# Kernel optimization log

Hardware: AMD Instinct MI355X
Metric: run time of the kernel (lower is better)

Reference implementation:

```python
import jax, jax.numpy as jnp
import numpy as np
import math

SPARSITY = 0.5
EPS = 1e-5


def _quant(x, bit, after_relu):
    # mirrors torch quantize_per_tensor math; straight-through (torch mutates x.data)
    def q(x):
        mx, mn = x.max(), x.min()
        scale = (mx - mn) / (2 ** bit - 1)
        if after_relu:
            ir = jnp.clip(jnp.round(x / scale), 0.0, 2 ** bit - 1)
            return ir * scale
        zp_min = jnp.floor(mn / scale)
        return (jnp.round((x - mn) / scale) + zp_min) * scale
    return x + jax.lax.stop_gradient(q(x) - x)


def _subnet(scores, k):
    # GetSubnet: top-k mask of |scores| with straight-through gradient
    s = jnp.abs(scores)
    flat = s.ravel()
    j = int((1.0 - k) * flat.size)
    order = jnp.argsort(flat)
    mask = jnp.zeros_like(flat).at[order[j:]].set(1.0).reshape(s.shape)
    return jax.lax.stop_gradient(mask - s) + s


def _scale(hw_one, fan_in):
    std = math.sqrt(2.0) / math.sqrt(fan_in * 0.5)
    return hw_one.mean() / std


def _blend_w(scores, sign, hw_one, hw_zero):
    m = _subnet(scores, SPARSITY)
    return sign * (hw_one[0] * m + hw_zero[0] * (1.0 - m))


def _conv(x, w):
    return jax.lax.conv_general_dilated(x, w, (1, 1), 'VALID',
                                        dimension_numbers=('NCHW', 'OIHW', 'NCHW'))


def _maxpool2(x):
    return jax.lax.reduce_window(x, -jnp.inf, jax.lax.max,
                                 (1, 1, 2, 2), (1, 1, 2, 2), 'VALID')


def _bn(x):
    m = x.mean((0, 2, 3), keepdims=True)
    v = x.var((0, 2, 3), keepdims=True)
    return (x - m) / jnp.sqrt(v + EPS)


def setup_inputs() -> dict:
    key = jax.random.key(0)
    ks = jax.random.split(key, 16)
    B = 4096
    shapes = {
        '1': (64, 1, 3, 3),
        '2': (16, 64, 3, 3),
        '3': (128, 400),
        '4': (10, 128),
    }
    inp = {'x': jax.random.normal(ks[0], (B, 1, 28, 28), dtype=jnp.float32)}
    i = 1
    for name, shp in shapes.items():
        inp['scores' + name] = jax.random.normal(ks[i], shp, dtype=jnp.float32); i += 1
        inp['sign' + name] = jnp.sign(jax.random.normal(ks[i], shp, dtype=jnp.float32)); i += 1
        inp['hw' + name + '_one'] = jax.random.uniform(ks[i], (1,) + shp, dtype=jnp.float32); i += 1
        # hw_zero: small "off" conductances
        inp['hw' + name + '_zero'] = 0.05 * jax.random.uniform(jax.random.fold_in(ks[i], 1), (1,) + shp, dtype=jnp.float32)
    inp['qb'] = 8
    return inp


def reference(x, scores1, sign1, hw1_one, hw1_zero,
              scores2, sign2, hw2_one, hw2_zero,
              scores3, sign3, hw3_one, hw3_zero,
              scores4, sign4, hw4_one, hw4_zero, qb):
    x = _maxpool2(x)
    x = _quant(x, qb, False)
    # conv1 (fan_in = 1*3*3 = 9)
    w1 = _blend_w(scores1, sign1, hw1_one, hw1_zero)
    x = _conv(x, w1) / _scale(hw1_one, 9)
    x = jax.nn.relu(_bn(x))
    x = _quant(x, qb, True)
    # conv2 (fan_in = 64*9 = 576)
    w2 = _blend_w(scores2, sign2, hw2_one, hw2_zero)
    x = _conv(x, w2) / _scale(hw2_one, 576)
    x = _maxpool2(x)
    x = jax.nn.relu(_bn(x))
    x = _quant(x, qb, True)
    x = x.reshape(x.shape[0], -1)  # [B, 400]
    # fc1 (fan_in = 400)
    w3 = _blend_w(scores3, sign3, hw3_one, hw3_zero)
    x = (x @ w3.T) / _scale(hw3_one, 400)
    x = jax.nn.relu(x)
    x = _quant(x, qb, True)
    # fc2 (fan_in = 128)
    w4 = _blend_w(scores4, sign4, hw4_one, hw4_zero)
    x = (x @ w4.T) / _scale(hw4_one, 128)
    return jax.nn.log_softmax(x, axis=1)
```

## Files before the change

### kernel.cpp

```cpp
#include <hip/hip_runtime.h>
#include <hip/hip_bf16.h>
#include <math.h>

#define DEV __device__ __forceinline__

constexpr int BATCH = 4096;
constexpr int NBA = 512;
constexpr int NBB = 1024;
constexpr int NBC = 4096;
constexpr int NBE = 512;
constexpr int NBW = 16;

constexpr size_t OFF_POOLED = 0;
constexpr size_t OFF_Y2P = OFF_POOLED + (size_t)BATCH*196;
constexpr size_t OFF_ST1 = OFF_Y2P;
constexpr size_t OFF_H3  = OFF_Y2P + (size_t)BATCH*400;
constexpr size_t OFF_ST2 = OFF_H3;
constexpr size_t OFF_W2  = OFF_H3 + (size_t)BATCH*128;
constexpr size_t OFF_W3  = OFF_W2 + 9216;
constexpr size_t OFF_W4  = OFF_W3 + 51200;
constexpr size_t OFF_WSC = OFF_W4 + 1280;
constexpr size_t OFF_BN1 = OFF_WSC + 4;
constexpr size_t OFF_BN2 = OFF_BN1 + 256;
constexpr size_t OFF_GMM = OFF_BN2 + 64;
constexpr size_t OFF_ONS = OFF_GMM + 8;
constexpr size_t OFF_T   = OFF_ONS + 16;
constexpr size_t OFF_MMA = OFF_T + 4;
constexpr size_t OFF_HIST= OFF_MMA + 1024;
constexpr size_t OFF_W1M = OFF_HIST + 32768;
constexpr size_t OFF_SEL = OFF_W1M + 2048;
constexpr size_t OFF_H2G = OFF_SEL + 8;
constexpr size_t OFF_H3G = OFF_H2G + 4096;

typedef __attribute__((ext_vector_type(8))) short bf16x8;
typedef __attribute__((ext_vector_type(4))) float f32x4;

struct InPtrs {
  const float* x;
  const float* sc[4];
  const float* sg[4];
  const float* on[4];
  const float* ze[4];
  const int* qb;
};

__constant__ const int KW_L[16]  ={0,1,1,2,2,2,2,2,2,2,2,2,2,2,2,3};
__constant__ const int KW_S[16]  ={0,0,1,0,1,2,3,4,5,6,7,8,9,10,11,0};
__constant__ const int KW_NB[4]  ={1,2,12,1};
__constant__ const int KW_N[4]   ={576,9216,51200,1280};
__constant__ const int KW_FAN[4] ={9,576,400,128};
__constant__ const int KW_BW0[4] ={0,1,3,15};
__constant__ const int KW_BW1[4] ={1,3,15,16};

DEV unsigned fenc(float f){ unsigned u=__float_as_uint(f); return (u&0x80000000u)? ~u : (u|0x80000000u); }
DEV float fdec(unsigned e){ return __uint_as_float((e&0x80000000u)? (e&0x7fffffffu) : ~e); }
DEV unsigned short f2bf(float f){ unsigned u=__float_as_uint(f); return (unsigned short)((u + 0x7fffu + ((u>>16)&1u))>>16); }

DEV float blk_sum(float v, float* red, int t){
  red[t]=v; __syncthreads();
  for (int s=128;s>0;s>>=1){ if(t<s) red[t]+=red[t+s]; __syncthreads(); }
  float r=red[0]; __syncthreads();
  return r;
}
DEV float blk_min(float v, float* red, int t){
  red[t]=v; __syncthreads();
  for (int s=128;s>0;s>>=1){ if(t<s) red[t]=fminf(red[t],red[t+s]); __syncthreads(); }
  float r=red[0]; __syncthreads();
  return r;
}
DEV float blk_max(float v, float* red, int t){
  red[t]=v; __syncthreads();
  for (int s=128;s>0;s>>=1){ if(t<s) red[t]=fmaxf(red[t],red[t+s]); __syncthreads(); }
  float r=red[0]; __syncthreads();
  return r;
}

DEV int2 find256(const int* hist, int nbins, int kk, int t, int* suf, int* sh2){
  const int G=nbins>>8;
  const int lo=t*G;
  int g=0;
  for (int b=0;b<G;++b) g+=hist[lo+b];
  suf[t]=g; __syncthreads();
  for (int s=1;s<256;s<<=1){
    int add=(t+s<256)?suf[t+s]:0;
    __syncthreads();
    suf[t]+=add;
    __syncthreads();
  }
  const int S=suf[t];
  const int Snext=(t<255)?suf[t+1]:0;
  if (S>=kk && Snext<kk){
    int c2=Snext;
    for (int b=lo+G-1;b>=lo;--b){
      c2+=hist[b];
      if (c2>=kk){ sh2[0]=b; sh2[1]=kk-(c2-hist[b]); break; }
    }
  }
  __syncthreads();
  int2 r=make_int2(sh2[0],sh2[1]);
  __syncthreads();
  return r;
}

DEV void build_pat(unsigned* PAT, const unsigned short* qxs, int t){
  for (int pos=t; pos<144; pos+=256){
    int py=(pos*171)>>11;
    int px=pos-py*12;
    const unsigned short* q0=qxs+py*16+px;
    unsigned e0=q0[0],  e1=q0[1],  e2=q0[2];
    unsigned e3=q0[16], e4=q0[17], e5=q0[18];
    unsigned e6=q0[32], e7=q0[33], e8=q0[34];
    uint4* dst=(uint4*)(PAT+pos*20);
    dst[0]=make_uint4(e0|(e1<<16), e2|(e3<<16), e4|(e5<<16), e6|(e7<<16));
    dst[1]=make_uint4(e8, 0u, 0u, 0u);
    dst[2]=make_uint4(0u,0u,0u,0u);
    dst[3]=make_uint4(0u,0u,0u,0u);
  }
}

__global__ __launch_bounds__(256) void ka_kernel(InPtrs in, float* __restrict__ ws){
  const int t=threadIdx.x, blk=blockIdx.x;
  __shared__ int h[2048];
  __shared__ float red[256];
  if (blk<NBA){
    if (blk==0){
      unsigned* Z=(unsigned*)(ws+OFF_H2G);
      for (int i=t;i<8192;i+=256) Z[i]=0u;
    }
    const float* x=in.x;
    float* pooled=ws+OFF_POOLED;
    float lmn=3.4e38f, lmx=-3.4e38f;
    if (t<196){
      const int oy=(t*2341)>>15;
      const int ox=t-oy*14;
      const float* xb=x+(size_t)blk*8*784+oy*56+ox*2;
      #pragma unroll
      for (int im=0; im<8; ++im){
        const float* px=xb+im*784;
        float m=fmaxf(fmaxf(px[0],px[1]),fmaxf(px[28],px[29]));
        pooled[(size_t)(blk*8+im)*196+t]=m;
        lmn=fminf(lmn,m); lmx=fmaxf(lmx,m);
      }
    }
    float bmn=blk_min(lmn,red,t);
    float bmx=blk_max(lmx,red,t);
    if (t==0){ ws[OFF_MMA+blk*2]=bmn; ws[OFF_MMA+blk*2+1]=bmx; }
  } else {
    const int bw=blk-NBA;
    const int L=KW_L[bw], s=KW_S[bw], nb=KW_NB[L];
    const int n4=KW_N[L]>>2;
    const int lo=(int)(((long long)n4*s)/nb), hi=(int)(((long long)n4*(s+1))/nb);
    const float4* sc4=(const float4*)in.sc[L];
    const float4* on4=(const float4*)in.on[L];
    for (int i=t;i<2048;i+=256) h[i]=0;
    __syncthreads();
    float onsum=0.f;
    for (int i=lo+t;i<hi;i+=256){
      float4 v=sc4[i];
      atomicAdd(&h[(__float_as_uint(v.x)&0x7fffffffu)>>20],1);
      atomicAdd(&h[(__float_as_uint(v.y)&0x7fffffffu)>>20],1);
      atomicAdd(&h[(__float_as_uint(v.z)&0x7fffffffu)>>20],1);
      atomicAdd(&h[(__float_as_uint(v.w)&0x7fffffffu)>>20],1);
      float4 o=on4[i];
      onsum+=(o.x+o.y)+(o.z+o.w);
    }
    __syncthreads();
    unsigned* GH=(unsigned*)(ws+OFF_HIST);
    for (int i=t;i<2048;i+=256) GH[bw*2048+i]=(unsigned)h[i];
    float S=blk_sum(onsum,red,t);
    if (t==0) ws[OFF_ONS+bw]=S;
  }
}

__global__ __launch_bounds__(256) void kw2a_kernel(float* __restrict__ ws){
  const int t=threadIdx.x, L=blockIdx.x;
  __shared__ int hist[2048];
  __shared__ int suf[256];
  __shared__ int sh2[2];
  __shared__ float redm[256], redx[256];
  if (L==0){
    float a0=ws[OFF_MMA+2*t],       a1=ws[OFF_MMA+2*(t+256)];
    float b0=ws[OFF_MMA+2*t+1],     b1=ws[OFF_MMA+2*(t+256)+1];
    redm[t]=fminf(a0,a1); redx[t]=fmaxf(b0,b1);
    __syncthreads();
    for (int s=128;s>0;s>>=1){
      if (t<s){ redm[t]=fminf(redm[t],redm[t+s]); redx[t]=fmaxf(redx[t],redx[t+s]); }
      __syncthreads();
    }
    unsigned* U=(unsigned*)(ws+OFF_GMM);
    if (t==0){ U[0]=fenc(redm[0]); U[1]=fenc(redx[0]); }
    if (t>=2 && t<8) U[t]=(t&1)? 0u : 0xFFFFFFFFu;
    unsigned* z=(unsigned*)(ws+OFF_W1M);
    for (int i=t;i<2048;i+=256) z[i]=0u;
    __syncthreads();
  }
  const unsigned* GH=(const unsigned*)(ws+OFF_HIST);
  for (int i=t;i<2048;i+=256){
    int s=0;
    for (int bw=KW_BW0[L]; bw<KW_BW1[L]; ++bw) s+=(int)GH[bw*2048+i];
    hist[i]=s;
  }
  __syncthreads();
  int2 f1=find256(hist,2048,KW_N[L]>>1,t,suf,sh2);
  if (t==0){
    unsigned* SEL=(unsigned*)(ws+OFF_SEL);
    SEL[L*2]=(unsigned)f1.x; SEL[L*2+1]=(unsigned)f1.y;
  }
}

__global__ __launch_bounds__(256) void kwp2_kernel(InPtrs in, float* __restrict__ ws){
  const int t=threadIdx.x, bw=blockIdx.x;
  const int L=KW_L[bw], s=KW_S[bw], nb=KW_NB[L];
  const int n4=KW_N[L]>>2;
  const int lo=(int)(((long long)n4*s)/nb), hi=(int)(((long long)n4*(s+1))/nb);
  const unsigned b0=((const unsigned*)(ws+OFF_SEL))[L*2];
  const float4* sc4=(const float4*)in.sc[L];
  unsigned* GH2=(unsigned*)(ws+OFF_H2G)+L*1024;
  for (int i=lo+t;i<hi;i+=256){
    float4 v=sc4[i];
    unsigned ux=__float_as_uint(v.x)&0x7fffffffu;
    unsigned uy=__float_as_uint(v.y)&0x7fffffffu;
    unsigned uz=__float_as_uint(v.z)&0x7fffffffu;
    unsigned uw=__float_as_uint(v.w)&0x7fffffffu;
    if ((ux>>20)==b0) atomicAdd(&GH2[(ux>>10)&1023u],1u);
    if ((uy>>20)==b0) atomicAdd(&GH2[(uy>>10)&1023u],1u);
    if ((uz>>20)==b0) atomicAdd(&GH2[(uz>>10)&1023u],1u);
    if ((uw>>20)==b0) atomicAdd(&GH2[(uw>>10)&1023u],1u);
  }
}

__global__ __launch_bounds__(256) void kwp3_kernel(InPtrs in, float* __restrict__ ws){
  const int t=threadIdx.x, bw=blockIdx.x;
  const int L=KW_L[bw], s=KW_S[bw], nb=KW_NB[L];
  const int n4=KW_N[L]>>2;
  const int lo=(int)(((long long)n4*s)/nb), hi=(int)(((long long)n4*(s+1))/nb);
  const unsigned* SEL=(const unsigned*)(ws+OFF_SEL);
  const unsigned b0=SEL[L*2]; const int r1=(int)SEL[L*2+1];
  __shared__ int hist[1024];
  __shared__ int suf[256];
  __shared__ int sh2[2];
  const unsigned* GH2=(const unsigned*)(ws+OFF_H2G)+L*1024;
  for (int i=t;i<1024;i+=256) hist[i]=(int)GH2[i];
  __syncthreads();
  int2 f2=find256(hist,1024,r1,t,suf,sh2);
  const unsigned pre=(b0<<10)|(unsigned)f2.x;
  const float4* sc4=(const float4*)in.sc[L];
  unsigned* GH3=(unsigned*)(ws+OFF_H3G)+L*1024;
  for (int i=lo+t;i<hi;i+=256){
    float4 v=sc4[i];
    unsigned ux=__float_as_uint(v.x)&0x7fffffffu;
    unsigned uy=__float_as_uint(v.y)&0x7fffffffu;
    unsigned uz=__float_as_uint(v.z)&0x7fffffffu;
    unsigned uw=__float_as_uint(v.w)&0x7fffffffu;
    if ((ux>>10)==pre) atomicAdd(&GH3[ux&1023u],1u);
    if ((uy>>10)==pre) atomicAdd(&GH3[uy&1023u],1u);
    if ((uz>>10)==pre) atomicAdd(&GH3[uz&1023u],1u);
    if ((uw>>10)==pre) atomicAdd(&GH3[uw&1023u],1u);
  }
}

__global__ __launch_bounds__(256) void kw3_kernel(InPtrs in, float* __restrict__ ws){
  const int t=threadIdx.x, bw=blockIdx.x;
  const int L=KW_L[bw], s=KW_S[bw], nb=KW_NB[L];
  const int n4=KW_N[L]>>2;
  const int lo=(int)(((long long)n4*s)/nb), hi=(int)(((long long)n4*(s+1))/nb);
  const unsigned* SEL=(const unsigned*)(ws+OFF_SEL);
  const unsigned b0=SEL[L*2]; const int r1=(int)SEL[L*2+1];
  __shared__ int hist[1024];
  __shared__ int suf[256];
  __shared__ int sh2[2];
  const unsigned* GH2=(const unsigned*)(ws+OFF_H2G)+L*1024;
  for (int i=t;i<1024;i+=256) hist[i]=(int)GH2[i];
  __syncthreads();
  int2 f2=find256(hist,1024,r1,t,suf,sh2);
  const unsigned pre=(b0<<10)|(unsigned)f2.x;
  const int r2=f2.y;
  __syncthreads();
  const unsigned* GH3=(const unsigned*)(ws+OFF_H3G)+L*1024;
  for (int i=t;i<1024;i+=256) hist[i]=(int)GH3[i];
  __syncthreads();
  int2 f3=find256(hist,1024,r2,t,suf,sh2);
  const unsigned T=(pre<<10)|(unsigned)f3.x;
  if (s==0 && t==0){
    float os=0.f;
    for (int b=KW_BW0[L]; b<KW_BW1[L]; ++b) os+=ws[OFF_ONS+b];
    ws[OFF_WSC+L]=(os/(float)KW_N[L])*sqrtf((float)KW_FAN[L])*0.5f;
  }
  const float4* sc4=(const float4*)in.sc[L];
  const float4* sg4=(const float4*)in.sg[L];
  const float4* on4=(const float4*)in.on[L];
  const float4* ze4=(const float4*)in.ze[L];
  float* wout=ws+OFF_W4;
  unsigned* W3Fu=(unsigned*)(ws+OFF_W3);
  unsigned short* W1F=(unsigned short*)(ws+OFF_W1M);
  unsigned short* W2F=(unsigned short*)(ws+OFF_W2);
  for (int i4=lo+t;i4<hi;i4+=256){
    float4 sv4=sc4[i4], g=sg4[i4], o=on4[i4], z=ze4[i4];
    float sv[4]={sv4.x,sv4.y,sv4.z,sv4.w}, gv[4]={g.x,g.y,g.z,g.w};
    float ov[4]={o.x,o.y,o.z,o.w}, zv[4]={z.x,z.y,z.z,z.w};
    #pragma unroll
    for (int j=0;j<4;++j){
      int i=i4*4+j;
      unsigned u=__float_as_uint(sv[j])&0x7fffffffu;
      float w=gv[j]*((u>=T)? ov[j] : zv[j]);
      if (L==0){
        int oc=i/9; int k=i-oc*9;
        int ocT=oc>>4, ocL=oc&15, quad=k>>3, kj=k&7;
        unsigned short hb=f2bf(w);
        float lo2=w-__uint_as_float((unsigned)hb<<16);
        W1F[((((ocT*2+0)*4+quad)*16+ocL)<<3)+kj]=hb;
        W1F[((((ocT*2+1)*4+quad)*16+ocL)<<3)+kj]=f2bf(lo2);
      } else if (L==1){
        int oc=i/576; int r=i-oc*576; int ic=r/9; int kp=r-ic*9;
        int ss=ic>>5, rem=ic&31, quad=rem>>3, kj=rem&7;
        unsigned short hb=f2bf(w);
        float lo2=w-__uint_as_float((unsigned)hb<<16);
        W2F[(((((kp*2+ss)*2+0)*4+quad)*16+oc)<<3)+kj]=hb;
        W2F[(((((kp*2+ss)*2+1)*4+quad)*16+oc)<<3)+kj]=f2bf(lo2);
      } else if (L==2){
        int oc=i/400; int kk=i-oc*400;
        unsigned short hb=f2bf(w);
        float lo2=w-__uint_as_float((unsigned)hb<<16);
        unsigned short lb=f2bf(lo2);
        int ct=oc>>4, l15=oc&15;
        unsigned idx=((unsigned)((kk>>4)*8+ct)*64u + (unsigned)(((kk>>2)&3)*16+l15))*4u + (unsigned)(kk&3);
        W3Fu[idx]=(unsigned)hb | ((unsigned)lb<<16);
      } else {
        wout[i]=w;
      }
    }
  }
}

__global__ __launch_bounds__(256) void kb_kernel(InPtrs in, const float* __restrict__ wsr, float* __restrict__ wsw){
  const int t=threadIdx.x, blk=blockIdx.x;
  __shared__ unsigned short qxs[256];
  __shared__ __align__(16) unsigned PAT[2880];
  __shared__ float xw[1024];
  const float* pooled=wsr+OFF_POOLED;
  const unsigned* U=(const unsigned*)(wsr+OFF_GMM);
  const float mn0=fdec(U[0]);
  const float mx0=fdec(U[1]);
  const float lvf=(float)((1<<in.qb[0])-1);
  const float s0=(mx0-mn0)/lvf, inv_s0=1.0f/s0, zp0=floorf(mn0/s0);
  const float sv=s0/wsr[OFF_WSC+0];
  const int w=t>>6, lane=t&63, l15=lane&15, quad=lane>>4;
  const unsigned short* W1F=(const unsigned short*)(wsr+OFF_W1M);
  bf16x8 bh[4], bl[4];
  #pragma unroll
  for (int ocT=0; ocT<4; ++ocT){
    bh[ocT]=*(const bf16x8*)(W1F+(((ocT*2+0)*64+lane)<<3));
    bl[ocT]=*(const bf16x8*)(W1F+(((ocT*2+1)*64+lane)<<3));
  }
  float sum[4], sq[4], mn[4], mx[4];
  #pragma unroll
  for (int i=0;i<4;++i){ sum[i]=0.f; sq[i]=0.f; mn[i]=3.4e38f; mx[i]=-3.4e38f; }
  for (int img=0; img<4; ++img){
    if (t<224){
      int row=t>>4, col=t&15;
      float q=0.f;
      if (col<14){ float xx=pooled[(size_t)(blk*4+img)*196+row*14+col]; q=rintf((xx-mn0)*inv_s0)+zp0; }
      qxs[t]=(unsigned short)(__float_as_uint(q)>>16);
    }
    __syncthreads();
    build_pat(PAT,qxs,t);
    __syncthreads();
    const unsigned short* PATu=(const unsigned short*)PAT;
    #pragma unroll
    for (int ocT=0; ocT<4; ++ocT){
      for (int tl=w; tl<9; tl+=4){
        bf16x8 a=*(const bf16x8*)(PATu+(tl*16+l15)*40+quad*8);
        f32x4 acc=(f32x4){0.f,0.f,0.f,0.f};
        acc=__builtin_amdgcn_mfma_f32_16x16x32_bf16(a,bh[ocT],acc,0,0,0);
        acc=__builtin_amdgcn_mfma_f32_16x16x32_bf16(a,bl[ocT],acc,0,0,0);
        #pragma unroll
        for (int r=0;r<4;++r){
          float v=acc[r];
          sum[ocT]+=v; sq[ocT]=fmaf(v,v,sq[ocT]);
          mn[ocT]=fminf(mn[ocT],v); mx[ocT]=fmaxf(mx[ocT],v);
        }
      }
    }
    __syncthreads();
  }
  #pragma unroll
  for (int ocT=0; ocT<4; ++ocT){
    float s=sum[ocT], q2=sq[ocT], a=mn[ocT], b=mx[ocT];
    #pragma unroll
    for (int d=16;d<64;d<<=1){
      s+=__shfl_xor(s,d);
      q2+=__shfl_xor(q2,d);
      a=fminf(a,__shfl_xor(a,d));
      b=fmaxf(b,__shfl_xor(b,d));
    }
    if (quad==0){
      float* p=xw+((w*4+ocT)*16+l15)*4;
      p[0]=s; p[1]=q2; p[2]=a; p[3]=b;
    }
  }
  __syncthreads();
  if (t<64){
    float s=0.f,q2=0.f,a=3.4e38f,b=-3.4e38f;
    #pragma unroll
    for (int w2=0;w2<4;++w2){
      const float* p=xw+((w2*4+(t>>4))*16+(t&15))*4;
      s+=p[0]; q2+=p[1]; a=fminf(a,p[2]); b=fmaxf(b,p[3]);
    }
    float* p=wsw+OFF_ST1+((size_t)t*NBB+blk)*4;
    p[0]=s*sv; p[1]=q2*sv*sv; p[2]=a*sv; p[3]=b*sv;
  }
}

__global__ __launch_bounds__(256) void kstat_kernel(const float* __restrict__ wsr, float* __restrict__ wsw,
                                                    unsigned long long inoff, int nparts, float Nf,
                                                    unsigned long long outoff, int mmslot){
  const int c=blockIdx.x, t=threadIdx.x;
  __shared__ float red[256];
  const float* p=wsr+inoff+(size_t)c*nparts*4;
  float sum=0.f,sq=0.f,mn=3.4e38f,mx=-3.4e38f;
  for (int i=t;i<nparts;i+=256){
    sum+=p[i*4]; sq+=p[i*4+1];
    mn=fminf(mn,p[i*4+2]); mx=fmaxf(mx,p[i*4+3]);
  }
  float S=blk_sum(sum,red,t);
  float Q=blk_sum(sq,red,t);
  float MN=blk_min(mn,red,t);
  float MX=blk_max(mx,red,t);
  if (t==0){
    float mean=S/Nf;
    float var=fmaxf(Q/Nf-mean*mean,0.f);
    float sd=sqrtf(var+1e-5f);
    float* o=wsw+outoff+c*4;
    float tmn=(MN-mean)/sd, tmx=(MX-mean)/sd;
    o[0]=mean; o[1]=sd; o[2]=tmn; o[3]=tmx;
    unsigned* U=(unsigned*)(wsw+OFF_GMM);
    atomicMin(&U[mmslot],fenc(tmn));
    atomicMax(&U[mmslot+1],fenc(tmx));
  }
}

__global__ __launch_bounds__(256) void kc_kernel(InPtrs in, const float* __restrict__ wsr, float* __restrict__ wsw){
  const int t=threadIdx.x, blk=blockIdx.x;
  __shared__ unsigned short qxs[256];
  __shared__ __align__(16) unsigned PATBUF[3328];
  __shared__ __align__(16) unsigned short actA[144*88];
  __shared__ float sA2[64], sB2[64];
  unsigned* PAT=PATBUF;
  float (*c2sP)[16][104]=(float(*)[16][104])PATBUF;
  const float* pooled=wsr+OFF_POOLED;
  const unsigned* U=(const unsigned*)(wsr+OFF_GMM);
  const float mn0=fdec(U[0]);
  const float mx0=fdec(U[1]);
  const float rmn=fdec(U[2]);
  const float rmx=fdec(U[3]);
  const float lvf=(float)((1<<in.qb[0])-1);
  const float s0=(mx0-mn0)/lvf, inv_s0=1.0f/s0, zp0=floorf(mn0/s0);
  const float s1w=wsr[OFF_WSC+0], s2w=wsr[OFF_WSC+1];
  const float s2=(fmaxf(rmx,0.f)-fmaxf(rmn,0.f))/lvf;
  const float inv_s2=1.0f/s2;
  const float g2=s2/s2w;
  if (t<64){
    float m=wsr[OFF_BN1+t*4], sd=wsr[OFF_BN1+t*4+1];
    sA2[t]=s0/(s1w*sd)*inv_s2;
    sB2[t]=(-m/sd)*inv_s2;
  }
  if (t<224){
    int row=t>>4, col=t&15;
    float q=0.f;
    if (col<14){ float xx=pooled[(size_t)blk*196+row*14+col]; q=rintf((xx-mn0)*inv_s0)+zp0; }
    qxs[t]=(unsigned short)(__float_as_uint(q)>>16);
  }
  __syncthreads();
  build_pat(PAT,qxs,t);
  __syncthreads();
  const int w=t>>6, lane=t&63;
  const int l15=lane&15, quad=lane>>4;
  {
    const unsigned short* W1F=(const unsigned short*)(wsr+OFF_W1M);
    const unsigned short* PATu=(const unsigned short*)PAT;
    #pragma unroll
    for (int ocT=0; ocT<4; ++ocT){
      bf16x8 bh=*(const bf16x8*)(W1F+(((ocT*2+0)*64+lane)<<3));
      bf16x8 bl=*(const bf16x8*)(W1F+(((ocT*2+1)*64+lane)<<3));
      const int oc0=ocT*16+quad*4;
      const float a20=sA2[oc0],   b20=sB2[oc0];
      const float a21=sA2[oc0+1], b21=sB2[oc0+1];
      const float a22=sA2[oc0+2], b22=sB2[oc0+2];
      const float a23=sA2[oc0+3], b23=sB2[oc0+3];
      for (int tl=w; tl<9; tl+=4){
        bf16x8 a=*(const bf16x8*)(PATu+(tl*16+l15)*40+quad*8);
        f32x4 acc=(f32x4){0.f,0.f,0.f,0.f};
        acc=__builtin_amdgcn_mfma_f32_16x16x32_bf16(bh,a,acc,0,0,0);
        acc=__builtin_amdgcn_mfma_f32_16x16x32_bf16(bl,a,acc,0,0,0);
        const int pos=tl*16+l15;
        float f0=fminf(rintf(fmaxf(fmaf(acc[0],a20,b20),0.f)),lvf);
        float f1=fminf(rintf(fmaxf(fmaf(acc[1],a21,b21),0.f)),lvf);
        float f2v=fminf(rintf(fmaxf(fmaf(acc[2],a22,b22),0.f)),lvf);
        float f3=fminf(rintf(fmaxf(fmaf(acc[3],a23,b23),0.f)),lvf);
        unsigned w0=(__float_as_uint(f0)>>16)|((__float_as_uint(f1)>>16)<<16);
        unsigned w1=(__float_as_uint(f2v)>>16)|((__float_as_uint(f3)>>16)<<16);
        *(uint2*)(actA+pos*88+oc0)=make_uint2(w0,w1);
      }
    }
  }
  __syncthreads();
  {
    const int wm=w>>1, wk=w&1;
    const int k0=wk?5:0, nK=wk?4:5;
    const int nT2=wm?3:4;
    const unsigned short* W2F=(const unsigned short*)(wsr+OFF_W2);
    int abase[4];
    #pragma unroll
    for (int i=0;i<4;++i){
      int tau=wm*4+i;
      int posb=tau*16+l15;
      int pc=posb>99?99:posb;
      int py=pc/10, px=pc-py*10;
      abase[i]=(py*12+px)*176+quad*16;
    }
    f32x4 acc[4];
    acc[0]=(f32x4){0.f,0.f,0.f,0.f};
    acc[1]=(f32x4){0.f,0.f,0.f,0.f};
    acc[2]=(f32x4){0.f,0.f,0.f,0.f};
    acc[3]=(f32x4){0.f,0.f,0.f,0.f};
    const char* actB=(const char*)actA;
    #pragma unroll
    for (int kk=0;kk<5;++kk){
      if (kk<nK){
        int kykx=k0+kk;
        int ky=(kykx*11)>>5;
        int kx=kykx-ky*3;
        int co=(ky*12+kx)*176;
        #pragma unroll
        for (int s=0;s<2;++s){
          bf16x8 bh=*(const bf16x8*)(W2F+((((kykx*2+s)*2+0)*64+lane)<<3));
          bf16x8 bl=*(const bf16x8*)(W2F+((((kykx*2+s)*2+1)*64+lane)<<3));
          #pragma unroll
          for (int i=0;i<4;++i){
            if (i<nT2){
              bf16x8 a=*(const bf16x8*)(actB+abase[i]+co+s*64);
              acc[i]=__builtin_amdgcn_mfma_f32_16x16x32_bf16(a,bh,acc[i],0,0,0);
              acc[i]=__builtin_amdgcn_mfma_f32_16x16x32_bf16(a,bl,acc[i],0,0,0);
            }
          }
        }
      }
    }
    #pragma unroll
    for (int i=0;i<4;++i){
      if (i<nT2){
        int pos4=(wm*4+i)*16+quad*4;
        if (pos4<100){
          float4* dst=(float4*)&c2sP[wk][l15][pos4];
          *dst=make_float4(acc[i].x*g2,acc[i].y*g2,acc[i].z*g2,acc[i].w*g2);
        }
      }
    }
  }
  __syncthreads();
  {
    const int ch=t>>4, g=t&15;
    const float* cc0=&c2sP[0][ch][0];
    const float* cc1=&c2sP[1][ch][0];
    float sum=0.f,sq=0.f,mn=3.4e38f,mx=-3.4e38f;
    #pragma unroll
    for (int it=0;it<2;++it){
      int j=g+it*16;
      if (j<25){
        int py=(j*52)>>8;
        int px=j-py*5;
        int base=py*20+px*2;
        float2 p0=*(const float2*)(cc0+base);
        float2 p1=*(const float2*)(cc0+base+10);
        float2 q0=*(const float2*)(cc1+base);
        float2 q1=*(const float2*)(cc1+base+10);
        float a0=p0.x+q0.x, a1=p0.y+q0.y;
        float b0=p1.x+q1.x, b1=p1.y+q1.y;
        float v=fmaxf(fmaxf(a0,a1),fmaxf(b0,b1));
        wsw[OFF_Y2P+(size_t)blk*400+ch*25+j]=v;
        sum+=v; sq=fmaf(v,v,sq); mn=fminf(mn,v); mx=fmaxf(mx,v);
      }
    }
    #pragma unroll
    for (int d=1;d<16;d<<=1){
      sum+=__shfl_xor(sum,d);
      sq +=__shfl_xor(sq,d);
      mn=fminf(mn,__shfl_xor(mn,d));
      mx=fmaxf(mx,__shfl_xor(mx,d));
    }
    if (g==0){
      float* p=wsw+OFF_ST2+((size_t)ch*NBC+blk)*4;
      p[0]=sum; p[1]=sq; p[2]=mn; p[3]=mx;
    }
  }
}

__global__ __launch_bounds__(256) void ke_kernel(InPtrs in, const float* __restrict__ wsr, float* __restrict__ wsw){
  const int t=threadIdx.x, blk=blockIdx.x;
  __shared__ __align__(16) unsigned short xs[16*808];
  __shared__ float sm[16], sisd[16];
  __shared__ float rwn[4], rwx[4];
  const unsigned* U=(const unsigned*)(wsr+OFF_GMM);
  const float lvf=(float)((1<<in.qb[0])-1);
  const float rmn=fdec(U[4]);
  const float rmx=fdec(U[5]);
  if (t<16){ sm[t]=wsr[OFF_BN2+t*4]; sisd[t]=1.0f/wsr[OFF_BN2+t*4+1]; }
  const float s3=(fmaxf(rmx,0.f)-fmaxf(rmn,0.f))/lvf;
  const float inv_s3=1.0f/s3;
  const float inv_s3w=1.0f/wsr[OFF_WSC+2];
  const int b0=(blk>>1)*16;
  __syncthreads();
  {
    const int img=t>>4, tg=t&15;
    const float* yrow=wsr+OFF_Y2P+(size_t)(b0+img)*400;
    unsigned* xsu=(unsigned*)xs;
    for (int n=0;n<25;++n){
      int k=n*16+tg;
      int ch=(k*5243)>>17;
      float y=yrow[k];
      float r=fmaxf((y-sm[ch])*sisd[ch],0.f);
      float q=fminf(rintf(r*inv_s3),lvf);
      unsigned qb=__float_as_uint(q)>>16;
      xsu[img*404+k]=qb|(qb<<16);
    }
  }
  __syncthreads();
  const int w=t>>6, lane=t&63, l15=lane&15, quad=lane>>4;
  const int ct=(blk&1)*4+w;
  const bf16x8* Wf=(const bf16x8*)(wsr+OFF_W3);
  const unsigned short* arow=xs+l15*808;
  f32x4 acc=(f32x4){0.f,0.f,0.f,0.f};
  #pragma unroll 5
  for (int kt=0;kt<25;++kt){
    bf16x8 a=*(const bf16x8*)(arow+kt*32+quad*8);
    bf16x8 b=Wf[(kt*8+ct)*64+lane];
    acc=__builtin_amdgcn_mfma_f32_16x16x32_bf16(a,b,acc,0,0,0);
  }
  const float scale=s3*inv_s3w;
  float hmn=3.4e38f,hmx=-3.4e38f;
  #pragma unroll
  for (int r=0;r<4;++r){
    float h=fmaxf(acc[r]*scale,0.f);
    wsw[OFF_H3+(size_t)(b0+quad*4+r)*128+ct*16+l15]=h;
    hmn=fminf(hmn,h); hmx=fmaxf(hmx,h);
  }
  #pragma unroll
  for (int d=1;d<64;d<<=1){
    hmn=fminf(hmn,__shfl_xor(hmn,d));
    hmx=fmaxf(hmx,__shfl_xor(hmx,d));
  }
  if (lane==0){ rwn[w]=hmn; rwx[w]=hmx; }
  __syncthreads();
  if (t==0){
    float mn=fminf(fminf(rwn[0],rwn[1]),fminf(rwn[2],rwn[3]));
    float mx=fmaxf(fmaxf(rwx[0],rwx[1]),fmaxf(rwx[2],rwx[3]));
    float* p=wsw+OFF_MMA+(size_t)blk*2;
    p[0]=mn; p[1]=mx;
  }
}

__global__ __launch_bounds__(256) void kf_kernel(InPtrs in, const float* __restrict__ wsr, float* __restrict__ out){
  const int t=threadIdx.x, blk=blockIdx.x;
  __shared__ float w4s[1280];
  __shared__ float redn[256], redxs[256];
  const float lvf=(float)((1<<in.qb[0])-1);
  for (int i=t;i<1280;i+=256) w4s[i]=wsr[OFF_W4+i];
  {
    const float* mmp=wsr+OFF_MMA;
    float mn=3.4e38f, mx=-3.4e38f;
    for (int i=t;i<NBE;i+=256){
      mn=fminf(mn,mmp[2*i]);
      mx=fmaxf(mx,mmp[2*i+1]);
    }
    redn[t]=mn; redxs[t]=mx;
    __syncthreads();
    for (int s=128;s>0;s>>=1){
      if (t<s){ redn[t]=fminf(redn[t],redn[t+s]); redxs[t]=fmaxf(redxs[t],redxs[t+s]); }
      __syncthreads();
    }
  }
  const float hmn=redn[0];
  const float hmx=redxs[0];
  const float s4=(hmx-hmn)/lvf;
  const float inv_s4=1.0f/s4;
  const float inv_s4w=1.0f/wsr[OFF_WSC+3];
  const int row=blk*64+(t>>2), l4=t&3;
  const float4* hr4=(const float4*)(wsr+OFF_H3+(size_t)row*128);
  float acc[10];
  #pragma unroll
  for (int j=0;j<10;++j) acc[j]=0.f;
  #pragma unroll 2
  for (int j=0;j<8;++j){
    float4 v=hr4[l4*8+j];
    int kb=(l4*8+j)*4;
    float q0=fminf(rintf(v.x*inv_s4),lvf)*s4;
    float q1=fminf(rintf(v.y*inv_s4),lvf)*s4;
    float q2=fminf(rintf(v.z*inv_s4),lvf)*s4;
    float q3=fminf(rintf(v.w*inv_s4),lvf)*s4;
    #pragma unroll
    for (int o=0;o<10;++o){
      const float* wr=w4s+o*128+kb;
      acc[o]=fmaf(q0,wr[0],acc[o]);
      acc[o]=fmaf(q1,wr[1],acc[o]);
      acc[o]=fmaf(q2,wr[2],acc[o]);
      acc[o]=fmaf(q3,wr[3],acc[o]);
    }
  }
  #pragma unroll
  for (int o=0;o<10;++o){
    acc[o]+=__shfl_xor(acc[o],1);
    acc[o]+=__shfl_xor(acc[o],2);
  }
  if (l4==0){
    float mx=-3.4e38f;
    #pragma unroll
    for (int o=0;o<10;++o){ acc[o]*=inv_s4w; mx=fmaxf(mx,acc[o]); }
    float se=0.f;
    #pragma unroll
    for (int o=0;o<10;++o) se+=expf(acc[o]-mx);
    const float ls=logf(se);
    #pragma unroll
    for (int o=0;o<10;++o) out[row*10+o]=acc[o]-mx-ls;
  }
}

extern "C" void kernel_launch(void* const* d_in, const int* in_sizes, int n_in,
                              void* d_out, int out_size, void* d_ws, size_t ws_size,
                              hipStream_t stream){
  (void)in_sizes; (void)n_in; (void)out_size; (void)ws_size;
  InPtrs P;
  P.x=(const float*)d_in[0];
  for (int l=0;l<4;++l){
    P.sc[l]=(const float*)d_in[1+l*4];
    P.sg[l]=(const float*)d_in[2+l*4];
    P.on[l]=(const float*)d_in[3+l*4];
    P.ze[l]=(const float*)d_in[4+l*4];
  }
  P.qb=(const int*)d_in[17];
  float* ws=(float*)d_ws;

  hipLaunchKernelGGL(ka_kernel,   dim3(NBA+NBW), dim3(256), 0, stream, P, ws);
  hipLaunchKernelGGL(kw2a_kernel, dim3(4),       dim3(256), 0, stream, ws);
  hipLaunchKernelGGL(kwp2_kernel, dim3(NBW),     dim3(256), 0, stream, P, ws);
  hipLaunchKernelGGL(kwp3_kernel, dim3(NBW),     dim3(256), 0, stream, P, ws);
  hipLaunchKernelGGL(kw3_kernel,  dim3(NBW),     dim3(256), 0, stream, P, ws);
  hipLaunchKernelGGL(kb_kernel,   dim3(NBB),     dim3(256), 0, stream, P, ws, ws);
  hipLaunchKernelGGL(kstat_kernel, dim3(64), dim3(256), 0, stream, ws, ws,
                     (unsigned long long)OFF_ST1, NBB, 4096.f*144.f, (unsigned long long)OFF_BN1, 2);
  hipLaunchKernelGGL(kc_kernel,   dim3(NBC),     dim3(256), 0, stream, P, ws, ws);
  hipLaunchKernelGGL(kstat_kernel, dim3(16), dim3(256), 0, stream, ws, ws,
                     (unsigned long long)OFF_ST2, NBC, 4096.f*25.f, (unsigned long long)OFF_BN2, 4);
  hipLaunchKernelGGL(ke_kernel,   dim3(NBE),     dim3(256), 0, stream, P, ws, ws);
  hipLaunchKernelGGL(kf_kernel,   dim3(64),      dim3(256), 0, stream, P, ws, (float*)d_out);
}
```

Measured before the change: 230.7 us.

## Fuse top-k selection kernels into one cooperative kernel and compact conv1 patch layout

```diff
diff --git a/kernel.cpp b/kernel.cpp
--- a/kernel.cpp
+++ b/kernel.cpp
@@ -1,6 +1,9 @@
 #include <hip/hip_runtime.h>
 #include <hip/hip_bf16.h>
+#include <hip/hip_cooperative_groups.h>
 #include <math.h>
+
+namespace cg = cooperative_groups;
 
 #define DEV __device__ __forceinline__
 
@@ -102,7 +105,7 @@
   return r;
 }
 
-DEV void build_pat(unsigned* PAT, const unsigned short* qxs, int t){
+DEV void build_patq(unsigned* PATQ, const unsigned short* qxs, int t){
   for (int pos=t; pos<144; pos+=256){
     int py=(pos*171)>>11;
     int px=pos-py*12;
@@ -110,11 +113,8 @@
     unsigned e0=q0[0],  e1=q0[1],  e2=q0[2];
     unsigned e3=q0[16], e4=q0[17], e5=q0[18];
     unsigned e6=q0[32], e7=q0[33], e8=q0[34];
-    uint4* dst=(uint4*)(PAT+pos*20);
-    dst[0]=make_uint4(e0|(e1<<16), e2|(e3<<16), e4|(e5<<16), e6|(e7<<16));
-    dst[1]=make_uint4(e8, 0u, 0u, 0u);
-    dst[2]=make_uint4(0u,0u,0u,0u);
-    dst[3]=make_uint4(0u,0u,0u,0u);
+    *(uint4*)(PATQ+pos*4)      =make_uint4(e0|(e1<<16), e2|(e3<<16), e4|(e5<<16), e6|(e7<<16));
+    *(uint4*)(PATQ+(144+pos)*4)=make_uint4(e8, 0u, 0u, 0u);
   }
 }
 
@@ -172,48 +172,50 @@
   }
 }
 
-__global__ __launch_bounds__(256) void kw2a_kernel(float* __restrict__ ws){
-  const int t=threadIdx.x, L=blockIdx.x;
+__global__ __launch_bounds__(256) void kwf_kernel(InPtrs in, float* __restrict__ ws){
+  const int t=threadIdx.x, bw=blockIdx.x;
   __shared__ int hist[2048];
   __shared__ int suf[256];
   __shared__ int sh2[2];
   __shared__ float redm[256], redx[256];
-  if (L==0){
-    float a0=ws[OFF_MMA+2*t],       a1=ws[OFF_MMA+2*(t+256)];
-    float b0=ws[OFF_MMA+2*t+1],     b1=ws[OFF_MMA+2*(t+256)+1];
-    redm[t]=fminf(a0,a1); redx[t]=fmaxf(b0,b1);
-    __syncthreads();
-    for (int s=128;s>0;s>>=1){
-      if (t<s){ redm[t]=fminf(redm[t],redm[t+s]); redx[t]=fmaxf(redx[t],redx[t+s]); }
+  cg::grid_group grid=cg::this_grid();
+  if (bw<4){
+    const int LA=bw;
+    if (LA==0){
+      float a0=ws[OFF_MMA+2*t],       a1=ws[OFF_MMA+2*(t+256)];
+      float b0v=ws[OFF_MMA+2*t+1],    b1v=ws[OFF_MMA+2*(t+256)+1];
+      redm[t]=fminf(a0,a1); redx[t]=fmaxf(b0v,b1v);
       __syncthreads();
-    }
-    unsigned* U=(unsigned*)(ws+OFF_GMM);
-    if (t==0){ U[0]=fenc(redm[0]); U[1]=fenc(redx[0]); }
-    if (t>=2 && t<8) U[t]=(t&1)? 0u : 0xFFFFFFFFu;
-    unsigned* z=(unsigned*)(ws+OFF_W1M);
-    for (int i=t;i<2048;i+=256) z[i]=0u;
-    __syncthreads();
-  }
-  const unsigned* GH=(const unsigned*)(ws+OFF_HIST);
-  for (int i=t;i<2048;i+=256){
-    int s=0;
-    for (int bw=KW_BW0[L]; bw<KW_BW1[L]; ++bw) s+=(int)GH[bw*2048+i];
-    hist[i]=s;
-  }
-  __syncthreads();
-  int2 f1=find256(hist,2048,KW_N[L]>>1,t,suf,sh2);
-  if (t==0){
-    unsigned* SEL=(unsigned*)(ws+OFF_SEL);
-    SEL[L*2]=(unsigned)f1.x; SEL[L*2+1]=(unsigned)f1.y;
-  }
-}
-
-__global__ __launch_bounds__(256) void kwp2_kernel(InPtrs in, float* __restrict__ ws){
-  const int t=threadIdx.x, bw=blockIdx.x;
+      for (int s=128;s>0;s>>=1){
+        if (t<s){ redm[t]=fminf(redm[t],redm[t+s]); redx[t]=fmaxf(redx[t],redx[t+s]); }
+        __syncthreads();
+      }
+      unsigned* U=(unsigned*)(ws+OFF_GMM);
+      if (t==0){ U[0]=fenc(redm[0]); U[1]=fenc(redx[0]); }
+      if (t>=2 && t<8) U[t]=(t&1)? 0u : 0xFFFFFFFFu;
+      unsigned* z=(unsigned*)(ws+OFF_W1M);
+      for (int i=t;i<2048;i+=256) z[i]=0u;
+      __syncthreads();
+    }
+    const unsigned* GH=(const unsigned*)(ws+OFF_HIST);
+    for (int i=t;i<2048;i+=256){
+      int sm=0;
+      for (int b2=KW_BW0[LA]; b2<KW_BW1[LA]; ++b2) sm+=(int)GH[b2*2048+i];
+      hist[i]=sm;
+    }
+    __syncthreads();
+    int2 f1=find256(hist,2048,KW_N[LA]>>1,t,suf,sh2);
+    if (t==0){
+      unsigned* SEL=(unsigned*)(ws+OFF_SEL);
+      SEL[LA*2]=(unsigned)f1.x; SEL[LA*2+1]=(unsigned)f1.y;
+    }
+  }
+  grid.sync();
   const int L=KW_L[bw], s=KW_S[bw], nb=KW_NB[L];
   const int n4=KW_N[L]>>2;
   const int lo=(int)(((long long)n4*s)/nb), hi=(int)(((long long)n4*(s+1))/nb);
-  const unsigned b0=((const unsigned*)(ws+OFF_SEL))[L*2];
+  const unsigned* SEL=(const unsigned*)(ws+OFF_SEL);
+  const unsigned b0=SEL[L*2]; const int r1=(int)SEL[L*2+1];
   const float4* sc4=(const float4*)in.sc[L];
   unsigned* GH2=(unsigned*)(ws+OFF_H2G)+L*1024;
   for (int i=lo+t;i<hi;i+=256){
@@ -227,24 +229,12 @@
     if ((uz>>20)==b0) atomicAdd(&GH2[(uz>>10)&1023u],1u);
     if ((uw>>20)==b0) atomicAdd(&GH2[(uw>>10)&1023u],1u);
   }
-}
-
-__global__ __launch_bounds__(256) void kwp3_kernel(InPtrs in, float* __restrict__ ws){
-  const int t=threadIdx.x, bw=blockIdx.x;
-  const int L=KW_L[bw], s=KW_S[bw], nb=KW_NB[L];
-  const int n4=KW_N[L]>>2;
-  const int lo=(int)(((long long)n4*s)/nb), hi=(int)(((long long)n4*(s+1))/nb);
-  const unsigned* SEL=(const unsigned*)(ws+OFF_SEL);
-  const unsigned b0=SEL[L*2]; const int r1=(int)SEL[L*2+1];
-  __shared__ int hist[1024];
-  __shared__ int suf[256];
-  __shared__ int sh2[2];
-  const unsigned* GH2=(const unsigned*)(ws+OFF_H2G)+L*1024;
+  grid.sync();
   for (int i=t;i<1024;i+=256) hist[i]=(int)GH2[i];
   __syncthreads();
   int2 f2=find256(hist,1024,r1,t,suf,sh2);
   const unsigned pre=(b0<<10)|(unsigned)f2.x;
-  const float4* sc4=(const float4*)in.sc[L];
+  const int r2=f2.y;
   unsigned* GH3=(unsigned*)(ws+OFF_H3G)+L*1024;
   for (int i=lo+t;i<hi;i+=256){
     float4 v=sc4[i];
@@ -257,26 +247,7 @@
     if ((uz>>10)==pre) atomicAdd(&GH3[uz&1023u],1u);
     if ((uw>>10)==pre) atomicAdd(&GH3[uw&1023u],1u);
   }
-}
-
-__global__ __launch_bounds__(256) void kw3_kernel(InPtrs in, float* __restrict__ ws){
-  const int t=threadIdx.x, bw=blockIdx.x;
-  const int L=KW_L[bw], s=KW_S[bw], nb=KW_NB[L];
-  const int n4=KW_N[L]>>2;
-  const int lo=(int)(((long long)n4*s)/nb), hi=(int)(((long long)n4*(s+1))/nb);
-  const unsigned* SEL=(const unsigned*)(ws+OFF_SEL);
-  const unsigned b0=SEL[L*2]; const int r1=(int)SEL[L*2+1];
-  __shared__ int hist[1024];
-  __shared__ int suf[256];
-  __shared__ int sh2[2];
-  const unsigned* GH2=(const unsigned*)(ws+OFF_H2G)+L*1024;
-  for (int i=t;i<1024;i+=256) hist[i]=(int)GH2[i];
-  __syncthreads();
-  int2 f2=find256(hist,1024,r1,t,suf,sh2);
-  const unsigned pre=(b0<<10)|(unsigned)f2.x;
-  const int r2=f2.y;
-  __syncthreads();
-  const unsigned* GH3=(const unsigned*)(ws+OFF_H3G)+L*1024;
+  grid.sync();
   for (int i=t;i<1024;i+=256) hist[i]=(int)GH3[i];
   __syncthreads();
   int2 f3=find256(hist,1024,r2,t,suf,sh2);
@@ -286,7 +257,6 @@
     for (int b=KW_BW0[L]; b<KW_BW1[L]; ++b) os+=ws[OFF_ONS+b];
     ws[OFF_WSC+L]=(os/(float)KW_N[L])*sqrtf((float)KW_FAN[L])*0.5f;
   }
-  const float4* sc4=(const float4*)in.sc[L];
   const float4* sg4=(const float4*)in.sg[L];
   const float4* on4=(const float4*)in.on[L];
   const float4* ze4=(const float4*)in.ze[L];
@@ -335,7 +305,7 @@
 __global__ __launch_bounds__(256) void kb_kernel(InPtrs in, const float* __restrict__ wsr, float* __restrict__ wsw){
   const int t=threadIdx.x, blk=blockIdx.x;
   __shared__ unsigned short qxs[256];
-  __shared__ __align__(16) unsigned PAT[2880];
+  __shared__ __align__(16) unsigned PAT[2304];
   __shared__ float xw[1024];
   const float* pooled=wsr+OFF_POOLED;
   const unsigned* U=(const unsigned*)(wsr+OFF_GMM);
@@ -352,6 +322,7 @@
     bh[ocT]=*(const bf16x8*)(W1F+(((ocT*2+0)*64+lane)<<3));
     bl[ocT]=*(const bf16x8*)(W1F+(((ocT*2+1)*64+lane)<<3));
   }
+  for (int i=1152+t; i<2304; i+=256) PAT[i]=0u;
   float sum[4], sq[4], mn[4], mx[4];
   #pragma unroll
   for (int i=0;i<4;++i){ sum[i]=0.f; sq[i]=0.f; mn[i]=3.4e38f; mx[i]=-3.4e38f; }
@@ -363,13 +334,13 @@
       qxs[t]=(unsigned short)(__float_as_uint(q)>>16);
     }
     __syncthreads();
-    build_pat(PAT,qxs,t);
+    build_patq(PAT,qxs,t);
     __syncthreads();
     const unsigned short* PATu=(const unsigned short*)PAT;
     #pragma unroll
     for (int ocT=0; ocT<4; ++ocT){
       for (int tl=w; tl<9; tl+=4){
-        bf16x8 a=*(const bf16x8*)(PATu+(tl*16+l15)*40+quad*8);
+        bf16x8 a=*(const bf16x8*)(PATu+((quad*144+tl*16+l15)<<3));
         f32x4 acc=(f32x4){0.f,0.f,0.f,0.f};
         acc=__builtin_amdgcn_mfma_f32_16x16x32_bf16(a,bh[ocT],acc,0,0,0);
         acc=__builtin_amdgcn_mfma_f32_16x16x32_bf16(a,bl[ocT],acc,0,0,0);
@@ -470,8 +441,9 @@
     if (col<14){ float xx=pooled[(size_t)blk*196+row*14+col]; q=rintf((xx-mn0)*inv_s0)+zp0; }
     qxs[t]=(unsigned short)(__float_as_uint(q)>>16);
   }
-  __syncthreads();
-  build_pat(PAT,qxs,t);
+  for (int i=1152+t; i<2304; i+=256) PAT[i]=0u;
+  __syncthreads();
+  build_patq(PAT,qxs,t);
   __syncthreads();
   const int w=t>>6, lane=t&63;
   const int l15=lane&15, quad=lane>>4;
@@ -488,7 +460,7 @@
       const float a22=sA2[oc0+2], b22=sB2[oc0+2];
       const float a23=sA2[oc0+3], b23=sB2[oc0+3];
       for (int tl=w; tl<9; tl+=4){
-        bf16x8 a=*(const bf16x8*)(PATu+(tl*16+l15)*40+quad*8);
+        bf16x8 a=*(const bf16x8*)(PATu+((quad*144+tl*16+l15)<<3));
         f32x4 acc=(f32x4){0.f,0.f,0.f,0.f};
         acc=__builtin_amdgcn_mfma_f32_16x16x32_bf16(bh,a,acc,0,0,0);
         acc=__builtin_amdgcn_mfma_f32_16x16x32_bf16(bl,a,acc,0,0,0);
@@ -740,10 +712,10 @@
   float* ws=(float*)d_ws;
 
   hipLaunchKernelGGL(ka_kernel,   dim3(NBA+NBW), dim3(256), 0, stream, P, ws);
-  hipLaunchKernelGGL(kw2a_kernel, dim3(4),       dim3(256), 0, stream, ws);
-  hipLaunchKernelGGL(kwp2_kernel, dim3(NBW),     dim3(256), 0, stream, P, ws);
-  hipLaunchKernelGGL(kwp3_kernel, dim3(NBW),     dim3(256), 0, stream, P, ws);
-  hipLaunchKernelGGL(kw3_kernel,  dim3(NBW),     dim3(256), 0, stream, P, ws);
+  {
+    void* kwfArgs[]={(void*)&P,(void*)&ws};
+    hipLaunchCooperativeKernel((const void*)kwf_kernel, dim3(NBW), dim3(256), kwfArgs, 0, stream);
+  }
   hipLaunchKernelGGL(kb_kernel,   dim3(NBB),     dim3(256), 0, stream, P, ws, ws);
   hipLaunchKernelGGL(kstat_kernel, dim3(64), dim3(256), 0, stream, ws, ws,
                      (unsigned long long)OFF_ST1, NBB, 4096.f*144.f, (unsigned long long)OFF_BN1, 2);
```

Result: slower. 280.4 us (+21.6%).
